# Kernel tuning notes

Hardware: AMD Instinct MI355X
Metric: run time of the kernel (lower is better)

Reference implementation:

```python
import jax, jax.numpy as jnp
import numpy as np

N = 4096       # num nodes == output_dim (delta is symmetrized NxN)
E = 65536      # num edges (avg degree 16)
IN_DIM = 128
H = 256        # hidden_dim (channels)
HEADS = 4


def setup_inputs():
    key = jax.random.key(0)
    ks = iter(jax.random.split(key, 40))
    def w(shape, s=0.05):
        return jax.random.normal(next(ks), shape, jnp.float32) * s
    inp = {}
    inp['x'] = jax.random.normal(next(ks), (N, IN_DIM), jnp.float32)
    inp['edge_index'] = jax.random.randint(next(ks), (2, E), 0, N)
    inp['pre_w'] = w((H, IN_DIM)); inp['pre_b'] = w((H,))
    for p in ('g1', 'g2'):
        inp[p + '_gcn_w'] = w((H, H)); inp[p + '_gcn_b'] = w((H,))
        inp[p + '_attn_in_w'] = w((3 * H, H)); inp[p + '_attn_in_b'] = w((3 * H,))
        inp[p + '_attn_out_w'] = w((H, H)); inp[p + '_attn_out_b'] = w((H,))
        inp[p + '_ffn_w1'] = w((2 * H, H)); inp[p + '_ffn_b1'] = w((2 * H,))
        inp[p + '_ffn_w2'] = w((H, 2 * H)); inp[p + '_ffn_b2'] = w((H,))
    inp['mlp_w1'] = w((H, H)); inp['mlp_b1'] = w((H,))
    inp['mlp_w2'] = w((N, H)); inp['mlp_b2'] = w((N,))
    return inp


def _gcn(x, src, dst, W, b):
    n = x.shape[0]
    x = x @ W.T
    loop = jnp.arange(n)
    s = jnp.concatenate([src, loop])
    d = jnp.concatenate([dst, loop])
    deg = jax.ops.segment_sum(jnp.ones(s.shape[0], x.dtype), d, num_segments=n)
    dinv = jnp.where(deg > 0, jax.lax.rsqrt(deg), 0.0)
    coef = (dinv[s] * dinv[d])[:, None]
    out = jax.ops.segment_sum(x[s] * coef, d, num_segments=n)
    return out + b


def _mha(h, in_w, in_b, out_w, out_b):
    # nn.MultiheadAttention self-attention over all N nodes (single dense graph)
    n, c = h.shape
    d = c // HEADS
    qkv = h @ in_w.T + in_b                      # [N, 3C]
    q, k, v = jnp.split(qkv, 3, axis=-1)
    q = q.reshape(n, HEADS, d).transpose(1, 0, 2) * (d ** -0.5)  # [h, n, d]
    k = k.reshape(n, HEADS, d).transpose(1, 0, 2)
    v = v.reshape(n, HEADS, d).transpose(1, 0, 2)
    a = jax.nn.softmax(jnp.einsum('hnd,hmd->hnm', q, k), axis=-1)
    o = jnp.einsum('hnm,hmd->hnd', a, v).transpose(1, 0, 2).reshape(n, c)
    return o @ out_w.T + out_b


def _gps(x, src, dst, gw, gb, iw, ib, ow, ob, w1, b1, w2, b2):
    # GPSConv, eval mode: dropout off, batch_norm (default running stats) = identity
    h1 = _gcn(x, src, dst, gw, gb) + x
    h2 = _mha(x, iw, ib, ow, ob) + x
    out = h1 + h2
    ff = jax.nn.relu(out @ w1.T + b1) @ w2.T + b2
    return out + ff


def reference(x, edge_index, pre_w, pre_b,
              g1_gcn_w, g1_gcn_b, g1_attn_in_w, g1_attn_in_b, g1_attn_out_w, g1_attn_out_b,
              g1_ffn_w1, g1_ffn_b1, g1_ffn_w2, g1_ffn_b2,
              g2_gcn_w, g2_gcn_b, g2_attn_in_w, g2_attn_in_b, g2_attn_out_w, g2_attn_out_b,
              g2_ffn_w1, g2_ffn_b1, g2_ffn_w2, g2_ffn_b2,
              mlp_w1, mlp_b1, mlp_w2, mlp_b2):
    src, dst = edge_index[0], edge_index[1]
    h = jax.nn.relu(x @ pre_w.T + pre_b)
    h = jax.nn.relu(_gps(h, src, dst, g1_gcn_w, g1_gcn_b, g1_attn_in_w, g1_attn_in_b,
                         g1_attn_out_w, g1_attn_out_b, g1_ffn_w1, g1_ffn_b1, g1_ffn_w2, g1_ffn_b2))
    h = jax.nn.relu(_gps(h, src, dst, g2_gcn_w, g2_gcn_b, g2_attn_in_w, g2_attn_in_b,
                         g2_attn_out_w, g2_attn_out_b, g2_ffn_w1, g2_ffn_b1, g2_ffn_w2, g2_ffn_b2))
    delta = jax.nn.relu(h @ mlp_w1.T + mlp_b1) @ mlp_w2.T + mlp_b2  # [N, N]
    return (delta + delta.T) * 0.5
```

## Files before the change

kernel.cpp:

```cpp
#include <hip/hip_runtime.h>

#define NN 4096
#define EE 65536
#define HC 256

typedef unsigned short ushort_t;
typedef __attribute__((ext_vector_type(8))) short bf16x8;
typedef __attribute__((ext_vector_type(4))) float f32x4;
typedef __attribute__((ext_vector_type(16))) float f32x16;

__device__ __forceinline__ ushort_t f2bf(float f) {
    unsigned int u = __float_as_uint(f);
    unsigned int r = (u + 0x7fffu + ((u >> 16) & 1u)) >> 16;
    return (ushort_t)r;
}
__device__ __forceinline__ float bf2f(ushort_t u) {
    return __uint_as_float(((unsigned int)u) << 16);
}
__device__ __forceinline__ unsigned int pack2bf(float a, float b) {
    unsigned int ua = __float_as_uint(a) + 0x8000u;
    unsigned int ub = __float_as_uint(b) + 0x8000u;
    return __builtin_amdgcn_perm(ub, ua, 0x07060302u);
}

__global__ void deg_init_k(float* __restrict__ deg) {
    int i = blockIdx.x * 256 + threadIdx.x;
    deg[i] = 1.0f;
}
__global__ void deg_scatter_k(const int* __restrict__ dst, float* __restrict__ deg) {
    int e = blockIdx.x * 256 + threadIdx.x;
    atomicAdd(&deg[dst[e]], 1.0f);
}
__global__ void dinv_k(const float* __restrict__ deg, float* __restrict__ dinv) {
    int i = blockIdx.x * 256 + threadIdx.x;
    dinv[i] = rsqrtf(deg[i]);
}
__global__ __launch_bounds__(1024)
void scan_offsets_k(const float* __restrict__ deg, int* __restrict__ offs,
                    int* __restrict__ cursor) {
    __shared__ int part[1024];
    const int t = threadIdx.x;
    int c0 = (int)deg[t * 4 + 0] - 1;
    int c1 = (int)deg[t * 4 + 1] - 1;
    int c2 = (int)deg[t * 4 + 2] - 1;
    int c3 = (int)deg[t * 4 + 3] - 1;
    part[t] = c0 + c1 + c2 + c3;
    __syncthreads();
    for (int off = 1; off < 1024; off <<= 1) {
        int v = (t >= off) ? part[t - off] : 0;
        __syncthreads();
        part[t] += v;
        __syncthreads();
    }
    int base = (t == 0) ? 0 : part[t - 1];
    offs[t * 4 + 0] = base;
    offs[t * 4 + 1] = base + c0;
    offs[t * 4 + 2] = base + c0 + c1;
    offs[t * 4 + 3] = base + c0 + c1 + c2;
    cursor[t * 4 + 0] = base;
    cursor[t * 4 + 1] = base + c0;
    cursor[t * 4 + 2] = base + c0 + c1;
    cursor[t * 4 + 3] = base + c0 + c1 + c2;
    if (t == 1023) offs[4096] = part[1023];
}
__global__ void csr_fill_k(const int* __restrict__ src, const int* __restrict__ dst,
                           int* __restrict__ cursor, int* __restrict__ csr_src) {
    int e = blockIdx.x * 256 + threadIdx.x;
    int pos = atomicAdd(&cursor[dst[e]], 1);
    csr_src[pos] = src[e];
}

__global__ __launch_bounds__(256)
void gcn_gather_k(const float* __restrict__ xw, const float* __restrict__ dinv,
                  const int* __restrict__ offs, const int* __restrict__ csr_src,
                  float* __restrict__ agg) {
    const int node = blockIdx.x * 4 + (threadIdx.x >> 6);
    const int c = (threadIdx.x & 63) * 4;
    const float dd = dinv[node];
    float4 a = *(const float4*)&xw[(size_t)node * HC + c];
    const float self = dd * dd;
    float4 acc = make_float4(a.x * self, a.y * self, a.z * self, a.w * self);
    const int beg = offs[node], end = offs[node + 1];
    for (int e = beg; e < end; e++) {
        int s = csr_src[e];
        float coef = dinv[s] * dd;
        const float4 v = *(const float4*)&xw[(size_t)s * HC + c];
        acc.x += v.x * coef;
        acc.y += v.y * coef;
        acc.z += v.z * coef;
        acc.w += v.w * coef;
    }
    *(float4*)&agg[(size_t)node * HC + c] = acc;
}

__global__ void cvt_bf16_k(const float* __restrict__ in, ushort_t* __restrict__ out) {
    int i = (blockIdx.x * 256 + threadIdx.x) * 4;
    float4 v = *(const float4*)&in[i];
    unsigned int d0 = pack2bf(v.x, v.y), d1 = pack2bf(v.z, v.w);
    *(uint2*)&out[i] = make_uint2(d0, d1);
}

__global__ __launch_bounds__(256)
void gemm_bf_k(const float* __restrict__ X, const float* __restrict__ W,
               const float* __restrict__ bias1, const float* __restrict__ bias2,
               const float* __restrict__ res1, const float* __restrict__ res2, float res2scale,
               float* __restrict__ out, int K, int M, int dorelu, int obf,
               int colsplit, const float* __restrict__ W2,
               const float* __restrict__ bias_r2, float* __restrict__ out2, int M2)
{
    __shared__ ushort_t As[64][72];
    __shared__ ushort_t Bs[32][72];
    const int t = threadIdx.x;
    const int w = t >> 6, lane = t & 63;
    const int m = lane & 15, quad = lane >> 4;
    const int row0 = blockIdx.y << 6, col0 = blockIdx.x << 5;
    const int sr = t >> 2;
    const int sc = (t & 3) << 4;
    const int wr2 = t >> 3;
    const int wc2 = (t & 7) << 3;

    const float* Wu = W;
    const float* b1u = bias1;
    const float* b2u = bias2;
    float* outu = out;
    int Mu = M, colu = col0;
    if (colsplit > 0 && col0 >= colsplit) {
        Wu = W2; b1u = bias_r2; b2u = nullptr;
        outu = out2; Mu = M2; colu = col0 - colsplit;
    }

    f32x4 acc[2] = {};
    for (int k0 = 0; k0 < K; k0 += 64) {
        const float* xp = &X[(size_t)(row0 + sr) * K + k0 + sc];
        const float* wp = &Wu[(size_t)(colu + wr2) * K + k0 + wc2];
        float4 xa = *(const float4*)xp,       xb = *(const float4*)(xp + 4);
        float4 xc = *(const float4*)(xp + 8), xd = *(const float4*)(xp + 12);
        float4 wa = *(const float4*)wp,       wb = *(const float4*)(wp + 4);
        __syncthreads();
        {
            unsigned int tx[8];
            tx[0] = pack2bf(xa.x, xa.y); tx[1] = pack2bf(xa.z, xa.w);
            tx[2] = pack2bf(xb.x, xb.y); tx[3] = pack2bf(xb.z, xb.w);
            tx[4] = pack2bf(xc.x, xc.y); tx[5] = pack2bf(xc.z, xc.w);
            tx[6] = pack2bf(xd.x, xd.y); tx[7] = pack2bf(xd.z, xd.w);
            *(uint4*)&As[sr][sc]     = *(const uint4*)&tx[0];
            *(uint4*)&As[sr][sc + 8] = *(const uint4*)&tx[4];
            unsigned int tw[4];
            tw[0] = pack2bf(wa.x, wa.y); tw[1] = pack2bf(wa.z, wa.w);
            tw[2] = pack2bf(wb.x, wb.y); tw[3] = pack2bf(wb.z, wb.w);
            *(uint4*)&Bs[wr2][wc2] = *(const uint4*)&tw[0];
        }
        __syncthreads();
        #pragma unroll
        for (int kc = 0; kc < 2; kc++) {
            bf16x8 af = *(const bf16x8*)&As[(w << 4) + m][kc * 32 + quad * 8];
            #pragma unroll
            for (int cb = 0; cb < 2; cb++) {
                bf16x8 bf = *(const bf16x8*)&Bs[cb * 16 + m][kc * 32 + quad * 8];
                acc[cb] = __builtin_amdgcn_mfma_f32_16x16x32_bf16(af, bf, acc[cb], 0, 0, 0);
            }
        }
    }
    #pragma unroll
    for (int cb = 0; cb < 2; cb++) {
        #pragma unroll
        for (int r = 0; r < 4; r++) {
            const int row = row0 + (w << 4) + quad * 4 + r;
            const int col = colu + cb * 16 + m;
            float v = acc[cb][r];
            if (b1u) v += b1u[col];
            if (b2u) v += b2u[col];
            if (res1) v += res1[(size_t)row * Mu + col];
            if (res2) v += res2scale * res2[(size_t)row * Mu + col];
            if (dorelu) v = fmaxf(v, 0.f);
            if (obf) ((ushort_t*)outu)[(size_t)row * Mu + col] = f2bf(v);
            else outu[(size_t)row * Mu + col] = v;
        }
    }
}

__global__ __launch_bounds__(256)
void kv_prep_k(const float* __restrict__ qkv, ushort_t* __restrict__ Kb,
               ushort_t* __restrict__ Vtb)
{
    __shared__ ushort_t Vs[64][72];
    const int h = blockIdx.y;
    const int n0 = blockIdx.x << 6;
    const int t = threadIdx.x;
    for (int u = t; u < 1024; u += 256) {
        int r = u >> 4, c = u & 15;
        const float* kp = &qkv[(size_t)(n0 + r) * 768 + 256 + h * 64 + c * 4];
        float4 kv = *(const float4*)kp;
        float4 vv = *(const float4*)(kp + 256);
        *(uint2*)&Kb[((size_t)(h * 4096 + n0 + r)) * 64 + c * 4] =
            make_uint2(pack2bf(kv.x, kv.y), pack2bf(kv.z, kv.w));
        *(uint2*)&Vs[r][c * 4] =
            make_uint2(pack2bf(vv.x, vv.y), pack2bf(vv.z, vv.w));
    }
    __syncthreads();
    int d = t >> 2, kc = t & 3;
    __attribute__((aligned(16))) ushort_t vals[16];
    #pragma unroll
    for (int k = 0; k < 16; k++) vals[k] = Vs[kc * 16 + k][d];
    ushort_t* op = &Vtb[((size_t)(h * 64 + d)) * 4096 + n0 + kc * 16];
    *(uint4*)op = *(const uint4*)&vals[0];
    *(uint4*)(op + 8) = *(const uint4*)&vals[8];
}

__global__ __launch_bounds__(256, 2)
void attn_part_k(const float* qkv, const ushort_t* __restrict__ Kb,
                 const ushort_t* __restrict__ Vtb, ushort_t* opart,
                 float* __restrict__ m_part, float* __restrict__ l_part)
{
    __shared__ ushort_t Kt[2][64][64];
    __shared__ ushort_t Vt[2][64][64];
    const int h = blockIdx.y & 3;
    const int split = blockIdx.y >> 2;
    const int q0 = blockIdx.x << 7;
    const int t = threadIdx.x;
    const int w = t >> 6;
    const int lane = t & 63;
    const int l31 = lane & 31;
    const int hi = lane >> 5;

    const int sr = t >> 3;
    const int sc = t & 7;
    const int swz = ((sc ^ (sr & 7)) << 3);
    const ushort_t* kp = &Kb[((size_t)(h * 4096 + split * 1024 + sr)) * 64 + sc * 8];
    const ushort_t* vp = &Vtb[((size_t)(h * 64 + sr)) * 4096 + split * 1024 + sc * 8];

    const float qs = 0.125f * 1.44269504f;
    const int qrow = q0 + w * 32 + l31;
    bf16x8 qf[4];
    #pragma unroll
    for (int s = 0; s < 4; s++) {
        const float* qp = &qkv[(size_t)qrow * 768 + h * 64 + s * 16 + hi * 8];
        float4 a = *(const float4*)qp;
        float4 b = *(const float4*)(qp + 4);
        union { uint4 u; bf16x8 v; } cv;
        cv.u = make_uint4(pack2bf(a.x * qs, a.y * qs), pack2bf(a.z * qs, a.w * qs),
                          pack2bf(b.x * qs, b.y * qs), pack2bf(b.z * qs, b.w * qs));
        qf[s] = cv.v;
    }

    f32x16 O0 = {}, O1 = {};
    float mrow = -1e30f;
    float ol = 0.f;

    uint4 ka0 = *(const uint4*)kp;
    uint4 ka1 = *(const uint4*)(kp + 32 * 64);
    uint4 va0 = *(const uint4*)vp;
    uint4 va1 = *(const uint4*)(vp + (size_t)32 * 4096);
    kp += 4096; vp += 64;
    *(uint4*)&Kt[0][sr][swz]      = ka0;
    *(uint4*)&Kt[0][sr + 32][swz] = ka1;
    *(uint4*)&Vt[0][sr][swz]      = va0;
    *(uint4*)&Vt[0][sr + 32][swz] = va1;
    ka0 = *(const uint4*)kp;
    ka1 = *(const uint4*)(kp + 32 * 64);
    va0 = *(const uint4*)vp;
    va1 = *(const uint4*)(vp + (size_t)32 * 4096);
    kp += 4096; vp += 64;
    asm volatile("s_waitcnt lgkmcnt(0)" ::: "memory");
    __builtin_amdgcn_s_barrier();

    for (int it = 0; it < 16; it++) {
        const int cur = it & 1;

        f32x16 S0 = {}, S1 = {};
        __builtin_amdgcn_s_setprio(1);
        #pragma unroll
        for (int s = 0; s < 4; s++) {
            const int cc = ((2 * s + hi) ^ (l31 & 7)) << 3;
            bf16x8 kf0 = *(const bf16x8*)&Kt[cur][l31][cc];
            bf16x8 kf1 = *(const bf16x8*)&Kt[cur][l31 + 32][cc];
            S0 = __builtin_amdgcn_mfma_f32_32x32x16_bf16(kf0, qf[s], S0, 0, 0, 0);
            S1 = __builtin_amdgcn_mfma_f32_32x32x16_bf16(kf1, qf[s], S1, 0, 0, 0);
        }
        __builtin_amdgcn_s_setprio(0);

        float r[32];
        #pragma unroll
        for (int i = 0; i < 16; i++) { r[i] = S0[i]; r[16 + i] = S1[i]; }
        #pragma unroll
        for (int st = 16; st > 0; st >>= 1)
            #pragma unroll
            for (int i = 0; i < st; i++) r[i] = fmaxf(r[i], r[i + st]);
        float mx = fmaxf(r[0], __shfl_xor(r[0], 32));

        if (__any(mx > mrow + 8.f)) {
            float mnew = fmaxf(mrow, mx);
            float alpha = __builtin_amdgcn_exp2f(mrow - mnew);
            mrow = mnew;
            ol *= alpha;
            #pragma unroll
            for (int rg = 0; rg < 16; rg++) {
                float ar = __shfl(alpha, (rg & 3) + 8 * (rg >> 2) + 4 * hi);
                O0[rg] *= ar;
                O1[rg] *= ar;
            }
        }

        #pragma unroll
        for (int i = 0; i < 16; i++) S0[i] = __builtin_amdgcn_exp2f(S0[i] - mrow);
        #pragma unroll
        for (int i = 0; i < 16; i++) S1[i] = __builtin_amdgcn_exp2f(S1[i] - mrow);

        float a2[32];
        #pragma unroll
        for (int i = 0; i < 16; i++) { a2[i] = S0[i]; a2[16 + i] = S1[i]; }
        #pragma unroll
        for (int st = 16; st > 0; st >>= 1)
            #pragma unroll
            for (int i = 0; i < st; i++) a2[i] += a2[i + st];
        ol += a2[0] + __shfl_xor(a2[0], 32);

        if (it < 15) {
            *(uint4*)&Kt[cur ^ 1][sr][swz]      = ka0;
            *(uint4*)&Kt[cur ^ 1][sr + 32][swz] = ka1;
            *(uint4*)&Vt[cur ^ 1][sr][swz]      = va0;
            *(uint4*)&Vt[cur ^ 1][sr + 32][swz] = va1;
            if (it < 14) {
                ka0 = *(const uint4*)kp;
                ka1 = *(const uint4*)(kp + 32 * 64);
                va0 = *(const uint4*)vp;
                va1 = *(const uint4*)(vp + (size_t)32 * 4096);
                kp += 4096; vp += 64;
            }
        }

        unsigned c[16], d[16];
        #pragma unroll
        for (int i = 0; i < 8; i++) c[i] = pack2bf(S0[2 * i], S0[2 * i + 1]);
        #pragma unroll
        for (int i = 0; i < 8; i++) c[8 + i] = pack2bf(S1[2 * i], S1[2 * i + 1]);
        #pragma unroll
        for (int i = 0; i < 16; i++) d[i] = __shfl_xor(c[i], 32);

        bf16x8 pa[4];
        #pragma unroll
        for (int b = 0; b < 2; b++) {
            union { uint4 u; bf16x8 v; } t0, t1;
            t0.u = make_uint4(hi ? d[8 * b + 2] : c[8 * b + 0],
                              hi ? d[8 * b + 3] : c[8 * b + 1],
                              hi ? c[8 * b + 2] : d[8 * b + 0],
                              hi ? c[8 * b + 3] : d[8 * b + 1]);
            t1.u = make_uint4(hi ? d[8 * b + 6] : c[8 * b + 4],
                              hi ? d[8 * b + 7] : c[8 * b + 5],
                              hi ? c[8 * b + 6] : d[8 * b + 4],
                              hi ? c[8 * b + 7] : d[8 * b + 5]);
            pa[2 * b] = t0.v;
            pa[2 * b + 1] = t1.v;
        }

        __builtin_amdgcn_s_setprio(1);
        #pragma unroll
        for (int ks = 0; ks < 4; ks++) {
            const int cc = ((2 * ks + hi) ^ (l31 & 7)) << 3;
            bf16x8 vf0 = *(const bf16x8*)&Vt[cur][l31][cc];
            bf16x8 vf1 = *(const bf16x8*)&Vt[cur][l31 + 32][cc];
            O0 = __builtin_amdgcn_mfma_f32_32x32x16_bf16(pa[ks], vf0, O0, 0, 0, 0);
            O1 = __builtin_amdgcn_mfma_f32_32x32x16_bf16(pa[ks], vf1, O1, 0, 0, 0);
        }
        __builtin_amdgcn_s_setprio(0);

        asm volatile("s_waitcnt lgkmcnt(0)" ::: "memory");
        __builtin_amdgcn_s_barrier();
    }

    #pragma unroll
    for (int rg = 0; rg < 16; rg++) {
        int q = q0 + w * 32 + (rg & 3) + 8 * (rg >> 2) + 4 * hi;
        size_t base = (size_t)q * 1536 + 512 + split * 256 + h * 64;
        opart[base + l31] = f2bf(O0[rg]);
        opart[base + 32 + l31] = f2bf(O1[rg]);
    }
    if (hi == 0) {
        m_part[(split * 4 + h) * 4096 + q0 + w * 32 + l31] = mrow;
        l_part[(split * 4 + h) * 4096 + q0 + w * 32 + l31] = ol;
    }
}

__global__ __launch_bounds__(256)
void attn_merge_k(const ushort_t* __restrict__ opart, const float* __restrict__ m_part,
                  const float* __restrict__ l_part, float* __restrict__ att)
{
    int idx = blockIdx.x * 256 + threadIdx.x;
    int q = idx >> 8, c = idx & 255;
    int h = c >> 6, d = c & 63;
    float ms[4];
    float mmax = -1e30f;
    #pragma unroll
    for (int s = 0; s < 4; s++) {
        ms[s] = m_part[(s * 4 + h) * 4096 + q];
        mmax = fmaxf(mmax, ms[s]);
    }
    float onum = 0.f, lden = 0.f;
    #pragma unroll
    for (int s = 0; s < 4; s++) {
        float wgt = __builtin_amdgcn_exp2f(ms[s] - mmax);
        float ov = bf2f(opart[(size_t)q * 1536 + 512 + s * 256 + h * 64 + d]);
        onum += wgt * ov;
        lden += wgt * l_part[(s * 4 + h) * 4096 + q];
    }
    att[(size_t)q * 256 + c] = onum / lden;
}

__global__ __launch_bounds__(256)
void sym_mlp_mfma_k(const ushort_t* __restrict__ Tb, const ushort_t* __restrict__ Wb,
                    const float* __restrict__ b2, float* __restrict__ out)
{
    __shared__ ushort_t As[128][72];
    __shared__ ushort_t Bs[128][72];
    const int t = threadIdx.x;
    const int w = t >> 6, lane = t & 63;
    const int m = lane & 15, quad = lane >> 4;
    const int wr = (w >> 1) * 64, wc = (w & 1) * 64;
    const int ri = blockIdx.y * 128, rj = blockIdx.x * 128;

    f32x4 acc[4][4] = {};
    for (int kk = 0; kk < 8; kk++) {
        const int k0 = kk * 64;
        const ushort_t* Asrc = (k0 < 256) ? Tb : Wb;
        const ushort_t* Bsrc = (k0 < 256) ? Wb : Tb;
        const int kcol = k0 & 255;
        __syncthreads();
        #pragma unroll
        for (int i = 0; i < 4; i++) {
            int s = t + i * 256;
            int row = s >> 3, ch = (s & 7) * 8;
            *(uint4*)&As[row][ch] = *(const uint4*)&Asrc[(size_t)(ri + row) * 256 + kcol + ch];
            *(uint4*)&Bs[row][ch] = *(const uint4*)&Bsrc[(size_t)(rj + row) * 256 + kcol + ch];
        }
        __syncthreads();
        #pragma unroll
        for (int kc = 0; kc < 2; kc++) {
            bf16x8 af[4], bfr[4];
            #pragma unroll
            for (int rb = 0; rb < 4; rb++)
                af[rb] = *(const bf16x8*)&As[wr + rb * 16 + m][kc * 32 + quad * 8];
            #pragma unroll
            for (int cb = 0; cb < 4; cb++)
                bfr[cb] = *(const bf16x8*)&Bs[wc + cb * 16 + m][kc * 32 + quad * 8];
            #pragma unroll
            for (int rb = 0; rb < 4; rb++)
                #pragma unroll
                for (int cb = 0; cb < 4; cb++)
                    acc[rb][cb] = __builtin_amdgcn_mfma_f32_16x16x32_bf16(af[rb], bfr[cb], acc[rb][cb], 0, 0, 0);
        }
    }
    #pragma unroll
    for (int rb = 0; rb < 4; rb++) {
        #pragma unroll
        for (int r = 0; r < 4; r++) {
            const int gr = ri + wr + rb * 16 + quad * 4 + r;
            const float br = b2[gr];
            #pragma unroll
            for (int cb = 0; cb < 4; cb++) {
                const int gc = rj + wc + cb * 16 + m;
                out[(size_t)gr * NN + gc] = 0.5f * (acc[rb][cb][r] + br + b2[gc]);
            }
        }
    }
}

extern "C" void kernel_launch(void* const* d_in, const int* in_sizes, int n_in,
                              void* d_out, int out_size, void* d_ws, size_t ws_size,
                              hipStream_t stream) {
    (void)in_sizes; (void)n_in; (void)out_size; (void)ws_size;
    const float* x = (const float*)d_in[0];
    const int* ei = (const int*)d_in[1];
    const int* src = ei;
    const int* dst = ei + EE;

    float* ws = (float*)d_ws;
    const int NH = NN * HC;
    float* h0  = ws;
    float* hb  = ws + 1 * NH;
    float* hc  = ws + 2 * NH;
    float* att = ws + 3 * NH;
    float* qkv = ws + 4 * NH;
    float* ffh = ws + 4 * NH;
    float* deg = ws + 7 * NH;
    float* dinv = deg + NN;
    int* offs    = (int*)(dinv + NN);
    int* cursor  = offs + 4100;
    int* csr_src = cursor + 4096;
    float* m_part = (float*)(csr_src + EE);
    float* l_part = m_part + 65536;
    ushort_t* Kb  = (ushort_t*)hc;
    ushort_t* Vtb = Kb + NH;
    ushort_t* Tb  = (ushort_t*)hb;
    ushort_t* W2b = Tb + NH;

    deg_init_k<<<NN / 256, 256, 0, stream>>>(deg);
    deg_scatter_k<<<EE / 256, 256, 0, stream>>>(dst, deg);
    dinv_k<<<NN / 256, 256, 0, stream>>>(deg, dinv);
    scan_offsets_k<<<1, 1024, 0, stream>>>(deg, offs, cursor);
    csr_fill_k<<<EE / 256, 256, 0, stream>>>(src, dst, cursor, csr_src);

    gemm_bf_k<<<dim3(8, 64), 256, 0, stream>>>(
        x, (const float*)d_in[2], (const float*)d_in[3], nullptr,
        nullptr, nullptr, 0.f, h0, 128, 256, 1, 0,
        0, nullptr, nullptr, nullptr, 0);

    for (int L = 0; L < 2; L++) {
        int B = 4 + L * 10;
        const float* gw = (const float*)d_in[B + 0];
        const float* gb = (const float*)d_in[B + 1];
        const float* iw = (const float*)d_in[B + 2];
        const float* ib = (const float*)d_in[B + 3];
        const float* ow = (const float*)d_in[B + 4];
        const float* ob = (const float*)d_in[B + 5];
        const float* w1 = (const float*)d_in[B + 6];
        const float* b1 = (const float*)d_in[B + 7];
        const float* w2 = (const float*)d_in[B + 8];
        const float* b2 = (const float*)d_in[B + 9];

        gemm_bf_k<<<dim3(32, 64), 256, 0, stream>>>(
            h0, gw, nullptr, nullptr, nullptr, nullptr, 0.f, att, 256, 256, 0, 0,
            256, iw, ib, qkv, 768);
        gcn_gather_k<<<NN / 4, 256, 0, stream>>>(att, dinv, offs, csr_src, hb);
        kv_prep_k<<<dim3(64, 4), 256, 0, stream>>>(qkv, Kb, Vtb);
        attn_part_k<<<dim3(32, 16), 256, 0, stream>>>(
            qkv, Kb, Vtb, (ushort_t*)qkv, m_part, l_part);
        attn_merge_k<<<NN, 256, 0, stream>>>(
            (const ushort_t*)qkv, m_part, l_part, att);
        gemm_bf_k<<<dim3(8, 64), 256, 0, stream>>>(
            att, ow, ob, gb, hb, h0, 2.0f, hc, 256, 256, 0, 0,
            0, nullptr, nullptr, nullptr, 0);
        gemm_bf_k<<<dim3(16, 64), 256, 0, stream>>>(
            hc, w1, b1, nullptr, nullptr, nullptr, 0.f, ffh, 256, 512, 1, 0,
            0, nullptr, nullptr, nullptr, 0);
        gemm_bf_k<<<dim3(8, 64), 256, 0, stream>>>(
            ffh, w2, b2, nullptr, hc, nullptr, 0.f, h0, 512, 256, 1, 0,
            0, nullptr, nullptr, nullptr, 0);
    }

    gemm_bf_k<<<dim3(8, 64), 256, 0, stream>>>(
        h0, (const float*)d_in[24], (const float*)d_in[25], nullptr,
        nullptr, nullptr, 0.f, (float*)Tb, 256, 256, 1, 1,
        0, nullptr, nullptr, nullptr, 0);
    cvt_bf16_k<<<NH / 1024, 256, 0, stream>>>((const float*)d_in[26], W2b);
    sym_mlp_mfma_k<<<dim3(32, 32), 256, 0, stream>>>(
        Tb, W2b, (const float*)d_in[27], (float*)d_out);
}
```

Baseline: 412.5 us.

## Raise attention occupancy: split keys eightfold, single LDS buffer, half-tile softmax

The split-K attention kernel now divides the 4096 keys into 8 splits of 512 instead of 4 of 1024, doubling the grid to 1024 blocks. It drops LDS double buffering in favour of a single K/V tile with register prefetch and two barriers per step. Each 64-key tile is processed as two 32-key halves to cut register pressure, with launch bounds raised to 4 blocks per SIMD. Partial outputs move to a dedicated workspace region, and the merge kernel now combines 8 partials, which adds merge traffic and removes the overlap that double buffering provided.

Measured after the change: 415.2 us. No clear change (+0.7%).

```diff
diff --git a/kernel.cpp b/kernel.cpp
--- a/kernel.cpp
+++ b/kernel.cpp
@@ -207,13 +207,13 @@
     *(uint4*)(op + 8) = *(const uint4*)&vals[8];
 }
 
-__global__ __launch_bounds__(256, 2)
+__global__ __launch_bounds__(256, 4)
 void attn_part_k(const float* qkv, const ushort_t* __restrict__ Kb,
-                 const ushort_t* __restrict__ Vtb, ushort_t* opart,
+                 const ushort_t* __restrict__ Vtb, ushort_t* __restrict__ opart,
                  float* __restrict__ m_part, float* __restrict__ l_part)
 {
-    __shared__ ushort_t Kt[2][64][64];
-    __shared__ ushort_t Vt[2][64][64];
+    __shared__ ushort_t Kt[64][64];
+    __shared__ ushort_t Vt[64][64];
     const int h = blockIdx.y & 3;
     const int split = blockIdx.y >> 2;
     const int q0 = blockIdx.x << 7;
@@ -226,8 +226,8 @@
     const int sr = t >> 3;
     const int sc = t & 7;
     const int swz = ((sc ^ (sr & 7)) << 3);
-    const ushort_t* kp = &Kb[((size_t)(h * 4096 + split * 1024 + sr)) * 64 + sc * 8];
-    const ushort_t* vp = &Vtb[((size_t)(h * 64 + sr)) * 4096 + split * 1024 + sc * 8];
+    const ushort_t* kp = &Kb[((size_t)(h * 4096 + split * 512 + sr)) * 64 + sc * 8];
+    const ushort_t* vp = &Vtb[((size_t)(h * 64 + sr)) * 4096 + split * 512 + sc * 8];
 
     const float qs = 0.125f * 1.44269504f;
     const int qrow = q0 + w * 32 + l31;
@@ -247,131 +247,112 @@
     float mrow = -1e30f;
     float ol = 0.f;
 
-    uint4 ka0 = *(const uint4*)kp;
-    uint4 ka1 = *(const uint4*)(kp + 32 * 64);
-    uint4 va0 = *(const uint4*)vp;
-    uint4 va1 = *(const uint4*)(vp + (size_t)32 * 4096);
-    kp += 4096; vp += 64;
-    *(uint4*)&Kt[0][sr][swz]      = ka0;
-    *(uint4*)&Kt[0][sr + 32][swz] = ka1;
-    *(uint4*)&Vt[0][sr][swz]      = va0;
-    *(uint4*)&Vt[0][sr + 32][swz] = va1;
-    ka0 = *(const uint4*)kp;
-    ka1 = *(const uint4*)(kp + 32 * 64);
-    va0 = *(const uint4*)vp;
-    va1 = *(const uint4*)(vp + (size_t)32 * 4096);
-    kp += 4096; vp += 64;
-    asm volatile("s_waitcnt lgkmcnt(0)" ::: "memory");
-    __builtin_amdgcn_s_barrier();
-
-    for (int it = 0; it < 16; it++) {
-        const int cur = it & 1;
-
-        f32x16 S0 = {}, S1 = {};
-        __builtin_amdgcn_s_setprio(1);
+    {
+        uint4 ka0 = *(const uint4*)kp;
+        uint4 ka1 = *(const uint4*)(kp + 32 * 64);
+        uint4 va0 = *(const uint4*)vp;
+        uint4 va1 = *(const uint4*)(vp + (size_t)32 * 4096);
+        kp += 4096; vp += 64;
+        *(uint4*)&Kt[sr][swz]      = ka0;
+        *(uint4*)&Kt[sr + 32][swz] = ka1;
+        *(uint4*)&Vt[sr][swz]      = va0;
+        *(uint4*)&Vt[sr + 32][swz] = va1;
+    }
+    __syncthreads();
+
+    uint4 ka0, ka1, va0, va1;
+    for (int it = 0; it < 8; it++) {
         #pragma unroll
-        for (int s = 0; s < 4; s++) {
-            const int cc = ((2 * s + hi) ^ (l31 & 7)) << 3;
-            bf16x8 kf0 = *(const bf16x8*)&Kt[cur][l31][cc];
-            bf16x8 kf1 = *(const bf16x8*)&Kt[cur][l31 + 32][cc];
-            S0 = __builtin_amdgcn_mfma_f32_32x32x16_bf16(kf0, qf[s], S0, 0, 0, 0);
-            S1 = __builtin_amdgcn_mfma_f32_32x32x16_bf16(kf1, qf[s], S1, 0, 0, 0);
-        }
-        __builtin_amdgcn_s_setprio(0);
-
-        float r[32];
-        #pragma unroll
-        for (int i = 0; i < 16; i++) { r[i] = S0[i]; r[16 + i] = S1[i]; }
-        #pragma unroll
-        for (int st = 16; st > 0; st >>= 1)
-            #pragma unroll
-            for (int i = 0; i < st; i++) r[i] = fmaxf(r[i], r[i + st]);
-        float mx = fmaxf(r[0], __shfl_xor(r[0], 32));
-
-        if (__any(mx > mrow + 8.f)) {
-            float mnew = fmaxf(mrow, mx);
-            float alpha = __builtin_amdgcn_exp2f(mrow - mnew);
-            mrow = mnew;
-            ol *= alpha;
-            #pragma unroll
-            for (int rg = 0; rg < 16; rg++) {
-                float ar = __shfl(alpha, (rg & 3) + 8 * (rg >> 2) + 4 * hi);
-                O0[rg] *= ar;
-                O1[rg] *= ar;
+        for (int hf = 0; hf < 2; hf++) {
+            f32x16 S = {};
+            __builtin_amdgcn_s_setprio(1);
+            #pragma unroll
+            for (int s = 0; s < 4; s++) {
+                const int cc = ((2 * s + hi) ^ (l31 & 7)) << 3;
+                bf16x8 kf = *(const bf16x8*)&Kt[32 * hf + l31][cc];
+                S = __builtin_amdgcn_mfma_f32_32x32x16_bf16(kf, qf[s], S, 0, 0, 0);
             }
-        }
-
-        #pragma unroll
-        for (int i = 0; i < 16; i++) S0[i] = __builtin_amdgcn_exp2f(S0[i] - mrow);
-        #pragma unroll
-        for (int i = 0; i < 16; i++) S1[i] = __builtin_amdgcn_exp2f(S1[i] - mrow);
-
-        float a2[32];
-        #pragma unroll
-        for (int i = 0; i < 16; i++) { a2[i] = S0[i]; a2[16 + i] = S1[i]; }
-        #pragma unroll
-        for (int st = 16; st > 0; st >>= 1)
-            #pragma unroll
-            for (int i = 0; i < st; i++) a2[i] += a2[i + st];
-        ol += a2[0] + __shfl_xor(a2[0], 32);
-
-        if (it < 15) {
-            *(uint4*)&Kt[cur ^ 1][sr][swz]      = ka0;
-            *(uint4*)&Kt[cur ^ 1][sr + 32][swz] = ka1;
-            *(uint4*)&Vt[cur ^ 1][sr][swz]      = va0;
-            *(uint4*)&Vt[cur ^ 1][sr + 32][swz] = va1;
-            if (it < 14) {
+            __builtin_amdgcn_s_setprio(0);
+
+            if (hf == 0 && it < 7) {
                 ka0 = *(const uint4*)kp;
                 ka1 = *(const uint4*)(kp + 32 * 64);
                 va0 = *(const uint4*)vp;
                 va1 = *(const uint4*)(vp + (size_t)32 * 4096);
                 kp += 4096; vp += 64;
             }
-        }
-
-        unsigned c[16], d[16];
-        #pragma unroll
-        for (int i = 0; i < 8; i++) c[i] = pack2bf(S0[2 * i], S0[2 * i + 1]);
-        #pragma unroll
-        for (int i = 0; i < 8; i++) c[8 + i] = pack2bf(S1[2 * i], S1[2 * i + 1]);
-        #pragma unroll
-        for (int i = 0; i < 16; i++) d[i] = __shfl_xor(c[i], 32);
-
-        bf16x8 pa[4];
-        #pragma unroll
-        for (int b = 0; b < 2; b++) {
-            union { uint4 u; bf16x8 v; } t0, t1;
-            t0.u = make_uint4(hi ? d[8 * b + 2] : c[8 * b + 0],
-                              hi ? d[8 * b + 3] : c[8 * b + 1],
-                              hi ? c[8 * b + 2] : d[8 * b + 0],
-                              hi ? c[8 * b + 3] : d[8 * b + 1]);
-            t1.u = make_uint4(hi ? d[8 * b + 6] : c[8 * b + 4],
-                              hi ? d[8 * b + 7] : c[8 * b + 5],
-                              hi ? c[8 * b + 6] : d[8 * b + 4],
-                              hi ? c[8 * b + 7] : d[8 * b + 5]);
-            pa[2 * b] = t0.v;
-            pa[2 * b + 1] = t1.v;
-        }
-
-        __builtin_amdgcn_s_setprio(1);
-        #pragma unroll
-        for (int ks = 0; ks < 4; ks++) {
-            const int cc = ((2 * ks + hi) ^ (l31 & 7)) << 3;
-            bf16x8 vf0 = *(const bf16x8*)&Vt[cur][l31][cc];
-            bf16x8 vf1 = *(const bf16x8*)&Vt[cur][l31 + 32][cc];
-            O0 = __builtin_amdgcn_mfma_f32_32x32x16_bf16(pa[ks], vf0, O0, 0, 0, 0);
-            O1 = __builtin_amdgcn_mfma_f32_32x32x16_bf16(pa[ks], vf1, O1, 0, 0, 0);
-        }
-        __builtin_amdgcn_s_setprio(0);
-
-        asm volatile("s_waitcnt lgkmcnt(0)" ::: "memory");
-        __builtin_amdgcn_s_barrier();
+
+            float r[8];
+            #pragma unroll
+            for (int i = 0; i < 8; i++) r[i] = fmaxf(S[i], S[i + 8]);
+            #pragma unroll
+            for (int st = 4; st > 0; st >>= 1)
+                #pragma unroll
+                for (int i = 0; i < st; i++) r[i] = fmaxf(r[i], r[i + st]);
+            float mx = fmaxf(r[0], __shfl_xor(r[0], 32));
+
+            if (__any(mx > mrow + 8.f)) {
+                float mnew = fmaxf(mrow, mx);
+                float alpha = __builtin_amdgcn_exp2f(mrow - mnew);
+                mrow = mnew;
+                ol *= alpha;
+                #pragma unroll
+                for (int rg = 0; rg < 16; rg++) {
+                    float ar = __shfl(alpha, (rg & 3) + 8 * (rg >> 2) + 4 * hi);
+                    O0[rg] *= ar;
+                    O1[rg] *= ar;
+                }
+            }
+
+            #pragma unroll
+            for (int i = 0; i < 16; i++) S[i] = __builtin_amdgcn_exp2f(S[i] - mrow);
+
+            float a2[8];
+            #pragma unroll
+            for (int i = 0; i < 8; i++) a2[i] = S[i] + S[i + 8];
+            #pragma unroll
+            for (int st = 4; st > 0; st >>= 1)
+                #pragma unroll
+                for (int i = 0; i < st; i++) a2[i] += a2[i + st];
+            ol += a2[0] + __shfl_xor(a2[0], 32);
+
+            unsigned c[8], d[8];
+            #pragma unroll
+            for (int i = 0; i < 8; i++) c[i] = pack2bf(S[2 * i], S[2 * i + 1]);
+            #pragma unroll
+            for (int i = 0; i < 8; i++) d[i] = __shfl_xor(c[i], 32);
+
+            __builtin_amdgcn_s_setprio(1);
+            #pragma unroll
+            for (int j = 0; j < 2; j++) {
+                union { uint4 u; bf16x8 v; } pj;
+                pj.u = make_uint4(hi ? d[4 * j + 2] : c[4 * j + 0],
+                                  hi ? d[4 * j + 3] : c[4 * j + 1],
+                                  hi ? c[4 * j + 2] : d[4 * j + 0],
+                                  hi ? c[4 * j + 3] : d[4 * j + 1]);
+                const int cc = ((4 * hf + 2 * j + hi) ^ (l31 & 7)) << 3;
+                bf16x8 vf0 = *(const bf16x8*)&Vt[l31][cc];
+                bf16x8 vf1 = *(const bf16x8*)&Vt[l31 + 32][cc];
+                O0 = __builtin_amdgcn_mfma_f32_32x32x16_bf16(pj.v, vf0, O0, 0, 0, 0);
+                O1 = __builtin_amdgcn_mfma_f32_32x32x16_bf16(pj.v, vf1, O1, 0, 0, 0);
+            }
+            __builtin_amdgcn_s_setprio(0);
+        }
+
+        __syncthreads();
+        if (it < 7) {
+            *(uint4*)&Kt[sr][swz]      = ka0;
+            *(uint4*)&Kt[sr + 32][swz] = ka1;
+            *(uint4*)&Vt[sr][swz]      = va0;
+            *(uint4*)&Vt[sr + 32][swz] = va1;
+        }
+        __syncthreads();
     }
 
     #pragma unroll
     for (int rg = 0; rg < 16; rg++) {
         int q = q0 + w * 32 + (rg & 3) + 8 * (rg >> 2) + 4 * hi;
-        size_t base = (size_t)q * 1536 + 512 + split * 256 + h * 64;
+        size_t base = (size_t)q * 2048 + split * 256 + h * 64;
         opart[base + l31] = f2bf(O0[rg]);
         opart[base + 32 + l31] = f2bf(O1[rg]);
     }
@@ -388,18 +369,18 @@
     int idx = blockIdx.x * 256 + threadIdx.x;
     int q = idx >> 8, c = idx & 255;
     int h = c >> 6, d = c & 63;
-    float ms[4];
+    float ms[8];
     float mmax = -1e30f;
     #pragma unroll
-    for (int s = 0; s < 4; s++) {
+    for (int s = 0; s < 8; s++) {
         ms[s] = m_part[(s * 4 + h) * 4096 + q];
         mmax = fmaxf(mmax, ms[s]);
     }
     float onum = 0.f, lden = 0.f;
     #pragma unroll
-    for (int s = 0; s < 4; s++) {
+    for (int s = 0; s < 8; s++) {
         float wgt = __builtin_amdgcn_exp2f(ms[s] - mmax);
-        float ov = bf2f(opart[(size_t)q * 1536 + 512 + s * 256 + h * 64 + d]);
+        float ov = bf2f(opart[(size_t)q * 2048 + s * 256 + h * 64 + d]);
         onum += wgt * ov;
         lden += wgt * l_part[(s * 4 + h) * 4096 + q];
     }
@@ -487,11 +468,12 @@
     int* cursor  = offs + 4100;
     int* csr_src = cursor + 4096;
     float* m_part = (float*)(csr_src + EE);
-    float* l_part = m_part + 65536;
+    float* l_part = m_part + 131072;
     ushort_t* Kb  = (ushort_t*)hc;
     ushort_t* Vtb = Kb + NH;
     ushort_t* Tb  = (ushort_t*)hb;
     ushort_t* W2b = Tb + NH;
+    ushort_t* opart = (ushort_t*)(ws + 8 * (size_t)NH);
 
     deg_init_k<<<NN / 256, 256, 0, stream>>>(deg);
     deg_scatter_k<<<EE / 256, 256, 0, stream>>>(dst, deg);
@@ -522,10 +504,10 @@
             256, iw, ib, qkv, 768);
         gcn_gather_k<<<NN / 4, 256, 0, stream>>>(att, dinv, offs, csr_src, hb);
         kv_prep_k<<<dim3(64, 4), 256, 0, stream>>>(qkv, Kb, Vtb);
-        attn_part_k<<<dim3(32, 16), 256, 0, stream>>>(
-            qkv, Kb, Vtb, (ushort_t*)qkv, m_part, l_part);
+        attn_part_k<<<dim3(32, 32), 256, 0, stream>>>(
+            qkv, Kb, Vtb, opart, m_part, l_part);
         attn_merge_k<<<NN, 256, 0, stream>>>(
-            (const ushort_t*)qkv, m_part, l_part, att);
+            opart, m_part, l_part, att);
         gemm_bf_k<<<dim3(8, 64), 256, 0, stream>>>(
             att, ow, ob, gb, hb, h0, 2.0f, hc, 256, 256, 0, 0,
             0, nullptr, nullptr, nullptr, 0);
```
